# Performance work log

Measured on AMD Instinct MI355X. Metric: run time of the kernel, lower is better.

## Reference

```python
import jax, jax.numpy as jnp
import numpy as np

NH = 1024
NV = 31
LAYERS = 2
BS = 64
SEQ = 512
EPS = 1e-5


def _gru_layer(x_seq, h0, Wih, Whh, bih, bhh):
    """x_seq: [B,S,in], h0: [B,nh]. PyTorch GRU gate math. Returns [B,S,nh], h_last."""
    # Precompute input-side gates for all timesteps: [B,S,3nh]
    xg = jnp.einsum('bsi,gi->bsg', x_seq, Wih) + bih
    xg = jnp.swapaxes(xg, 0, 1)  # [S,B,3nh] for scan over time

    def step(h, xg_t):
        hg = h @ Whh.T + bhh  # [B,3nh]
        xr, xz, xn = jnp.split(xg_t, 3, axis=-1)
        hr, hz, hn = jnp.split(hg, 3, axis=-1)
        r = jax.nn.sigmoid(xr + hr)
        z = jax.nn.sigmoid(xz + hz)
        n = jnp.tanh(xn + r * hn)
        h_new = (1.0 - z) * n + z * h
        return h_new, h_new

    h_last, ys = jax.lax.scan(step, h0, xg)
    return jnp.swapaxes(ys, 0, 1), h_last  # [B,S,nh]


def setup_inputs() -> dict:
    key = jax.random.key(0)
    ks = jax.random.split(key, 16)
    s = 0.02
    inp = {
        'x': jax.random.randint(ks[0], (BS, SEQ), 0, NV),
        'h0': jnp.zeros((LAYERS, BS, NH), jnp.float32),
        'emb': jax.random.normal(ks[1], (NV, NH), jnp.float32) * s,
        'Wih0': jax.random.normal(ks[2], (3 * NH, NH), jnp.float32) * s,
        'Whh0': jax.random.normal(ks[3], (3 * NH, NH), jnp.float32) * s,
        'bih0': jnp.zeros((3 * NH,), jnp.float32),
        'bhh0': jnp.zeros((3 * NH,), jnp.float32),
        'Wih1': jax.random.normal(ks[4], (3 * NH, NH), jnp.float32) * s,
        'Whh1': jax.random.normal(ks[5], (3 * NH, NH), jnp.float32) * s,
        'bih1': jnp.zeros((3 * NH,), jnp.float32),
        'bhh1': jnp.zeros((3 * NH,), jnp.float32),
        'gamma': jnp.ones((NH,), jnp.float32),
        'beta': jnp.zeros((NH,), jnp.float32),
        'Wout': jax.random.normal(ks[6], (NV, NH), jnp.float32) * s,
        'bout': jnp.zeros((NV,), jnp.float32),
    }
    return inp


def reference(x, h0, emb, Wih0, Whh0, bih0, bhh0, Wih1, Whh1, bih1, bhh1,
              gamma, beta, Wout, bout):
    e = emb[x]  # [B,S,nh] embedding lookup
    y0, _ = _gru_layer(e, h0[0], Wih0, Whh0, bih0, bhh0)
    y1, _ = _gru_layer(y0, h0[1], Wih1, Whh1, bih1, bhh1)
    # BatchNorm1dFlat: flatten (B*S, nh), batch-statistics BN, reshape back
    flat = y1.reshape(-1, NH)
    mu = flat.mean(axis=0)
    var = flat.var(axis=0)  # biased, as in BN training
    bn = (y1 - mu) * jax.lax.rsqrt(var + EPS) * gamma + beta
    return bn @ Wout.T + bout  # [B,S,nv]
```

## Files before the change

### kernel.cpp

```cpp
#include <hip/hip_runtime.h>
#include <cstddef>
#include <stdint.h>

#define NHID 1024
#define NVOC 31
#define NB   64
#define NSEQ 512
#define NWRK 192
#define NGRID 256
#define NTHR 512
#define EPSV 1e-5f
#define RS2  36
#define SL   (NB*NHID)
#define XG_SLOTS 16

typedef __attribute__((ext_vector_type(8))) short short8;
typedef __attribute__((ext_vector_type(4))) float float4v;

#define OFF_F0  0
#define OFF_F1  4096
#define OFF_F2  8192
#define OFF_FIN 12288
#define CNT_BYTES 12352

#define M_OFF_Y0  12544
#define M_OFF_Y1  (M_OFF_Y0 + 513ull*SL*2)
#define M_OFF_H1I (M_OFF_Y1 + 512ull*SL*2)
#define M_OFF_T0  (M_OFF_H1I + (unsigned long long)SL*2)
#define M_OFF_ST  (M_OFF_T0 + 31ull*3*NHID*4)
#define M_OFF_XG  (M_OFF_ST + 16384ull)

#define LDS_BYTES 65024

__device__ __forceinline__ unsigned short f2bf(float f){
  unsigned u = __builtin_bit_cast(unsigned, f);
  u += 0x7fffu + ((u >> 16) & 1u);
  return (unsigned short)(u >> 16);
}
__device__ __forceinline__ float bf2f(unsigned short h){
  unsigned u = ((unsigned)h) << 16;
  return __builtin_bit_cast(float, u);
}
__device__ __forceinline__ float sigm(float x){ return 1.f/(1.f + __expf(-x)); }
__device__ __forceinline__ float tanh_f(float x){ return 1.f - 2.f/(__expf(2.f*x) + 1.f); }

__device__ __forceinline__ void burn(float& d){
#pragma unroll
  for (int i=0;i<16;++i)
    asm volatile("v_fmac_f32 %0, %1, %2" : "+v"(d) : "v"(d), "v"(d));
}

__device__ __forceinline__ void setflag(unsigned* f, unsigned v){
  __hip_atomic_store(f, v, __ATOMIC_RELAXED, __HIP_MEMORY_SCOPE_AGENT);
}
__device__ __forceinline__ void waitflags4(const unsigned* f, int base4, int target, int lane, float& d){
  const unsigned* p = f + (size_t)(base4 + (lane & 3))*16;
  for(;;){
    int v = (int)__hip_atomic_load(p, __ATOMIC_RELAXED, __HIP_MEMORY_SCOPE_AGENT);
    if (__all(v >= target)) break;
    burn(d);
  }
  asm volatile("" ::: "memory");
}
__device__ __forceinline__ void waitflag1(const unsigned* f, int idx, int target, float& d){
  const unsigned* p = f + (size_t)idx*16;
  while ((int)__hip_atomic_load(p, __ATOMIC_RELAXED, __HIP_MEMORY_SCOPE_AGENT) < target)
    burn(d);
  asm volatile("" ::: "memory");
}
__device__ __forceinline__ void waitflag1_slow(const unsigned* f, int idx, int target, float& d){
  const unsigned* p = f + (size_t)idx*16;
  while ((int)__hip_atomic_load(p, __ATOMIC_RELAXED, __HIP_MEMORY_SCOPE_AGENT) < target){
    burn(d); burn(d); burn(d); burn(d);
  }
  asm volatile("" ::: "memory");
}
__device__ __forceinline__ void sig(unsigned* c){
  __hip_atomic_fetch_add(c, 1u, __ATOMIC_RELAXED, __HIP_MEMORY_SCOPE_AGENT);
}
__device__ __forceinline__ void waitc(unsigned* c, unsigned v, float& d){
  while (__hip_atomic_load(c, __ATOMIC_RELAXED, __HIP_MEMORY_SCOPE_AGENT) < v)
    burn(d);
}

__device__ __forceinline__ void stc16(void* p, short8 v){
  asm volatile("global_store_dwordx4 %0, %1, off sc1"
               :: "v"((unsigned long long)(uintptr_t)p), "v"(v) : "memory");
}
__device__ __forceinline__ void stc4(void* p, float v){
  asm volatile("global_store_dword %0, %1, off sc1"
               :: "v"((unsigned long long)(uintptr_t)p), "v"(v) : "memory");
}
__device__ __forceinline__ void drain_vm(){
  asm volatile("s_waitcnt vmcnt(0)" ::: "memory");
}

__device__ __forceinline__ void load_bfrags6(const float* W, int ch0,
                                             short8 (&bfr)[6][4], int lane, int wid)
{
  const int l15 = lane & 15, q = lane >> 4;
#pragma unroll
  for (int nt=0; nt<6; ++nt){
    int grow = (nt>>1)*NHID + ch0 + (nt&1)*16 + l15;
    const float* wp0 = W + (size_t)grow*NHID + wid*128 + q*8;
#pragma unroll
    for (int kt=0; kt<4; ++kt){
      const float* wp = wp0 + kt*32;
      short8 fr;
#pragma unroll
      for (int j=0;j<8;++j) fr[j] = (short)f2bf(wp[j]);
      bfr[nt][kt] = fr;
    }
  }
}
__device__ __forceinline__ void load_a2(const unsigned short* slab, int b0,
                                        short8 (&f)[2][4], int lane, int wid)
{
#pragma unroll
  for (int mt=0;mt<2;++mt){
    const short8* p = (const short8*)(slab + (size_t)(b0 + mt*16 + (lane&15))*NHID
                                      + wid*128 + (lane>>4)*8);
#pragma unroll
    for (int kt=0;kt<4;++kt) f[mt][kt] = p[kt*4];
  }
}
__device__ __forceinline__ void gemm2d(const short8 (&fA)[2][4],
                                       const short8 (&bfr)[6][4],
                                       float* red, int lane, int wid)
{
  const int l15 = lane & 15, q = lane >> 4;
  float4v acc[2][6];
#pragma unroll
  for (int mt=0; mt<2; ++mt)
#pragma unroll
    for (int nt=0; nt<6; ++nt) acc[mt][nt] = (float4v){0.f,0.f,0.f,0.f};
#pragma unroll
  for (int kt=0; kt<4; ++kt){
#pragma unroll
    for (int nt=0; nt<6; ++nt){
      acc[0][nt] = __builtin_amdgcn_mfma_f32_16x16x32_bf16(fA[0][kt], bfr[nt][kt], acc[0][nt],0,0,0);
      acc[1][nt] = __builtin_amdgcn_mfma_f32_16x16x32_bf16(fA[1][kt], bfr[nt][kt], acc[1][nt],0,0,0);
    }
  }
  if (wid >= 4){
#pragma unroll
    for (int mt=0; mt<2; ++mt)
#pragma unroll
      for (int nt=0; nt<6; ++nt){
        int n = nt*16 + l15, row = mt*16 + q*4;
        *(float4v*)(red + ((wid-4)*96 + n)*RS2 + row) = acc[mt][nt];
      }
  }
  __syncthreads();
  if (wid < 4){
#pragma unroll
    for (int mt=0; mt<2; ++mt)
#pragma unroll
      for (int nt=0; nt<6; ++nt){
        int n = nt*16 + l15, row = mt*16 + q*4;
        float4v* p = (float4v*)(red + (wid*96 + n)*RS2 + row);
        float4v v = *p;
        *p = v + acc[mt][nt];
      }
  }
  __syncthreads();
}

__global__ __launch_bounds__(NTHR, 2) void mgru_fused(
    const int*   __restrict__ x,    const float* __restrict__ h0,
    const float* __restrict__ emb,
    const float* __restrict__ Wih0, const float* __restrict__ Whh0,
    const float* __restrict__ bih0, const float* __restrict__ bhh0,
    const float* __restrict__ Wih1, const float* __restrict__ Whh1,
    const float* __restrict__ bih1, const float* __restrict__ bhh1,
    const float* __restrict__ gamma, const float* __restrict__ beta,
    const float* __restrict__ Wout, const float* __restrict__ bout,
    float* __restrict__ out, char* ws)
{
  __shared__ __align__(16) char smem[LDS_BYTES];
  float* red = (float*)smem;

  unsigned* f0  = (unsigned*)(ws + OFF_F0);
  unsigned* f1  = (unsigned*)(ws + OFF_F1);
  unsigned* f2  = (unsigned*)(ws + OFF_F2);
  unsigned* fin = (unsigned*)(ws + OFF_FIN);
  unsigned short* y0b   = (unsigned short*)(ws + M_OFF_Y0);
  unsigned short* y1    = (unsigned short*)(ws + M_OFF_Y1);
  unsigned short* h1i   = (unsigned short*)(ws + M_OFF_H1I);
  float*          T0    = (float*)(ws + M_OFF_T0);
  float*          stats = (float*)(ws + M_OFF_ST);
  float*          xgring= (float*)(ws + M_OFF_XG);

  const int tid  = threadIdx.x;
  const int lane = tid & 63;
  const int wid  = tid >> 6;
  const int wg   = blockIdx.x;
  const int l15 = lane & 15, q = lane >> 4;
  float dummy = (float)tid * 1e-30f + 1.0f;

  if (wg >= NWRK){
    for(;;){
      for (int i=0;i<64;++i) burn(dummy);
      unsigned v = __hip_atomic_load(fin, __ATOMIC_RELAXED, __HIP_MEMORY_SCOPE_AGENT);
      if (v >= (unsigned)NWRK) break;
    }
    if (tid == 0) __threadfence();
    __syncthreads();
    if (dummy == 1234.5678f) ((volatile float*)smem)[0] = dummy;
    goto epilogue;
  }

  {
    if (tid == 0) __threadfence();
    __syncthreads();

    const int role = (wg < 64) ? 0 : (wg < 128 ? 1 : 2);

    if (role == 0){
      const int rw = wg, bg = rw >> 5, cg = rw & 31;
      const int b0 = bg*32, ch0 = cg*32;
      const int fidx = bg*32 + cg;
      const int g = tid;
      const int b = b0 + (g & 31);
      const int oct = g >> 5;
      short8 bfr0[6][4];
      float hprev[8] = {0,0,0,0,0,0,0,0};
      float br[8], bz[8], bn[8];

      if (tid < 128){
        short8 pk;
#pragma unroll
        for (int j=0;j<8;++j){
          int ch = ch0 + oct*8 + j;
          hprev[j] = h0[(size_t)b*NHID + ch];
          br[j] = bhh0[ch]; bz[j] = bhh0[NHID + ch]; bn[j] = bhh0[2*NHID + ch];
          pk[j] = (short)f2bf(hprev[j]);
        }
        stc16(y0b + (size_t)b*NHID + ch0 + oct*8, pk);
        drain_vm();
      }
      __syncthreads();
      if (tid == 0) setflag(f0 + (size_t)fidx*16, 1u);

      for (int e = tid; e < NVOC*96; e += NTHR){
        int v = e / 96, n = e - v*96;
        int gate = n >> 5, c32 = n & 31;
        int grow = gate*NHID + ch0 + c32;
        const float4v* e4 = (const float4v*)(emb  + (size_t)v*NHID);
        const float4v* w4 = (const float4v*)(Wih0 + (size_t)grow*NHID);
        float acc = 0.f;
        for (int k=0;k<NHID/4;++k){
          float4v a = e4[k], bb = w4[k];
          acc += a[0]*bb[0] + a[1]*bb[1] + a[2]*bb[2] + a[3]*bb[3];
        }
        T0[(size_t)v*3*NHID + grow] = acc + bih0[grow];
      }
      load_bfrags6(Whh0, ch0, bfr0, lane, wid);
      __syncthreads();

      for (int t = 0; t < NSEQ; ++t){
        waitflags4(f0, bg*32 + wid*4, t+1, lane, dummy);
        short8 fA[2][4];
        load_a2(y0b + (size_t)t*SL, b0, fA, lane, wid);
        gemm2d(fA, bfr0, red, lane, wid);
        if (tid < 128){
          int tok = x[(size_t)b*NSEQ + t];
          const float* tp = T0 + (size_t)tok*3*NHID;
          int m = g & 31;
          short8 pk;
#pragma unroll
          for (int j=0;j<8;++j){
            int c32 = oct*8 + j, ch = ch0 + c32;
            float hr = br[j], hz = bz[j], hn = bn[j];
#pragma unroll
            for (int w=0;w<4;++w){
              hr += red[(w*96 +      c32)*RS2 + m];
              hz += red[(w*96 + 32 + c32)*RS2 + m];
              hn += red[(w*96 + 64 + c32)*RS2 + m];
            }
            float r = sigm(tp[ch] + hr);
            float z = sigm(tp[NHID + ch] + hz);
            float n = tanh_f(tp[2*NHID + ch] + r*hn);
            float hnv = (1.f - z)*n + z*hprev[j];
            hprev[j] = hnv;
            pk[j] = (short)f2bf(hnv);
          }
          stc16(y0b + (size_t)(t+1)*SL + (size_t)b*NHID + ch0 + oct*8, pk);
          drain_vm();
        }
        __syncthreads();
        if (tid == 0) setflag(f0 + (size_t)fidx*16, (unsigned)(t+2));
      }

    } else if (role == 1){
      const int rw = wg - 64, bg = rw >> 5, cg = rw & 31;
      const int b0 = bg*32, ch0 = cg*32;
      const int fidx = bg*32 + cg;
      short8 wf[6][4];
      load_bfrags6(Wih1, ch0, wf, lane, wid);
      __syncthreads();

      for (int t = 0; t < NSEQ; ++t){
        if ((t & 3) == 0 && t >= 16)
          waitflag1_slow(f2, fidx, t-11, dummy);
        waitflags4(f0, bg*32 + wid*4, t+2, lane, dummy);
        short8 fB[2][4];
        load_a2(y0b + (size_t)(t+1)*SL, b0, fB, lane, wid);
        gemm2d(fB, wf, red, lane, wid);
        float* xgw = xgring + ((size_t)(t & (XG_SLOTS-1))*64 + (size_t)fidx)*3072;
#pragma unroll
        for (int i=0;i<6;++i){
          int idx = tid + i*512;
          int n = idx >> 5, m = idx & 31;
          float v = bih1[(n>>5)*NHID + ch0 + (n&31)];
          v += red[(      n)*RS2 + m];
          v += red[( 96 + n)*RS2 + m];
          v += red[(192 + n)*RS2 + m];
          v += red[(288 + n)*RS2 + m];
          stc4(xgw + idx, v);
        }
        drain_vm();
        __syncthreads();
        if (tid == 0) setflag(f1 + (size_t)fidx*16, (unsigned)(t+2));
      }

    } else {
      const int rw = wg - 128, bg = rw >> 5, cg = rw & 31;
      const int b0 = bg*32, ch0 = cg*32;
      const int fidx = bg*32 + cg;
      const int g = tid;
      const int b = b0 + (g & 31);
      const int oct = g >> 5;
      short8 bfrH[6][4];
      float hprev[8] = {0,0,0,0,0,0,0,0};
      float bhr[8], bhz[8], bhn[8];
      float s1[8] = {0,0,0,0,0,0,0,0}, s2[8] = {0,0,0,0,0,0,0,0};

      if (tid < 128){
        short8 pk;
#pragma unroll
        for (int j=0;j<8;++j){
          int ch = ch0 + oct*8 + j;
          hprev[j] = h0[(size_t)NB*NHID + (size_t)b*NHID + ch];
          bhr[j] = bhh1[ch]; bhz[j] = bhh1[NHID + ch]; bhn[j] = bhh1[2*NHID + ch];
          pk[j] = (short)f2bf(hprev[j]);
        }
        stc16(h1i + (size_t)b*NHID + ch0 + oct*8, pk);
        drain_vm();
      }
      __syncthreads();
      if (tid == 0) setflag(f2 + (size_t)fidx*16, 1u);

      load_bfrags6(Whh1, ch0, bfrH, lane, wid);
      __syncthreads();

      for (int t = 0; t < NSEQ; ++t){
        waitflags4(f2, bg*32 + wid*4, t+1, lane, dummy);
        const unsigned short* hsrc = (t == 0) ? h1i : (y1 + (size_t)(t-1)*SL);
        short8 fH[2][4];
        load_a2(hsrc, b0, fH, lane, wid);
        gemm2d(fH, bfrH, red, lane, wid);
        float hrv[8], hzv[8], hnv_[8];
        if (tid < 128){
          int m = g & 31;
#pragma unroll
          for (int j=0;j<8;++j){
            int c32 = oct*8 + j;
            float hr = bhr[j], hz = bhz[j], hn = bhn[j];
#pragma unroll
            for (int w=0;w<4;++w){
              hr += red[(w*96 +      c32)*RS2 + m];
              hz += red[(w*96 + 32 + c32)*RS2 + m];
              hn += red[(w*96 + 64 + c32)*RS2 + m];
            }
            hrv[j] = hr; hzv[j] = hz; hnv_[j] = hn;
          }
        }
        waitflag1(f1, fidx, t+2, dummy);
        if (tid < 128){
          const float* xgt = xgring + ((size_t)(t & (XG_SLOTS-1))*64 + (size_t)fidx)*3072;
          int m = g & 31;
          short8 pk;
#pragma unroll
          for (int j=0;j<8;++j){
            int c32 = oct*8 + j;
            float xr = __hip_atomic_load(xgt + (size_t)(     c32)*32 + m, __ATOMIC_RELAXED, __HIP_MEMORY_SCOPE_AGENT);
            float xz = __hip_atomic_load(xgt + (size_t)(32 + c32)*32 + m, __ATOMIC_RELAXED, __HIP_MEMORY_SCOPE_AGENT);
            float xn = __hip_atomic_load(xgt + (size_t)(64 + c32)*32 + m, __ATOMIC_RELAXED, __HIP_MEMORY_SCOPE_AGENT);
            float r  = sigm(xr + hrv[j]);
            float z  = sigm(xz + hzv[j]);
            float nn = tanh_f(xn + r*hnv_[j]);
            float hnew = (1.f - z)*nn + z*hprev[j];
            hprev[j] = hnew;
            unsigned short hb = f2bf(hnew);
            pk[j] = (short)hb;
            float hq = bf2f(hb);
            s1[j] += hq; s2[j] += hq*hq;
          }
          stc16(y1 + (size_t)t*SL + (size_t)b*NHID + ch0 + oct*8, pk);
          drain_vm();
        }
        __syncthreads();
        if (tid == 0) setflag(f2 + (size_t)fidx*16, (unsigned)(t+2));
      }

      {
        float* sb = (float*)smem;
        __syncthreads();
        if (tid < 128){
#pragma unroll
          for (int j=0;j<8;++j) sb[(oct*8 + j)*32 + (g & 31)] = s1[j];
        }
        __syncthreads();
        if (tid < 32){
          float a = 0.f;
          for (int i=0;i<32;++i) a += sb[tid*32 + i];
          stats[(size_t)bg*2048 + ch0 + tid] = a;
        }
        __syncthreads();
        if (tid < 128){
#pragma unroll
          for (int j=0;j<8;++j) sb[(oct*8 + j)*32 + (g & 31)] = s2[j];
        }
        __syncthreads();
        if (tid < 32){
          float a = 0.f;
          for (int i=0;i<32;++i) a += sb[tid*32 + i];
          stats[(size_t)bg*2048 + 1024 + ch0 + tid] = a;
        }
      }
    }

    __syncthreads();
    if (tid == 0){
      __threadfence();
      sig(fin);
      waitc(fin, NWRK, dummy);
      __threadfence();
    }
    __syncthreads();
    if (dummy == 1234.5678f) ((volatile float*)smem)[0] = dummy;
  }

epilogue:
  {
    const float inv_n = 1.f/32768.f;

    float* bpart    = (float*)smem;
    float* bprime_l = (float*)(smem + 2048);
    {
      int v = tid >> 4, k0 = tid & 15;
      float partial = 0.f;
      if (v < NVOC){
        for (int k = k0; k < NHID; k += 16){
          float s1k = stats[k] + stats[2048 + k];
          float s2k = stats[1024 + k] + stats[3072 + k];
          float mu  = s1k*inv_n;
          float var = s2k*inv_n - mu*mu;
          float sc  = gamma[k]*rsqrtf(var + EPSV);
          partial += (beta[k] - mu*sc) * Wout[(size_t)v*NHID + k];
        }
      }
      bpart[tid] = partial;
    }
    __syncthreads();
    if (tid < 32){
      float bpv = 0.f;
      for (int j=0;j<16;++j) bpv += bpart[tid*16 + j];
      bprime_l[tid] = (tid < NVOC) ? (bpv + bout[tid]) : 0.f;
    }
    __syncthreads();
    float bp_a = bprime_l[l15];
    float bp_b = (l15 < 15) ? bprime_l[16 + l15] : 0.f;
    __syncthreads();

    unsigned short* wsc = (unsigned short*)smem;
    for (int e = tid; e < NVOC*1032; e += NTHR){
      int v = e / 1032, k = e - v*1032;
      float val = 0.f;
      if (k < NHID){
        float s1k = stats[k] + stats[2048 + k];
        float s2k = stats[1024 + k] + stats[3072 + k];
        float mu  = s1k*inv_n;
        float var = s2k*inv_n - mu*mu;
        float sc  = gamma[k]*rsqrtf(var + EPSV);
        val = Wout[(size_t)v*NHID + k] * sc;
      }
      wsc[e] = f2bf(val);
    }
    __syncthreads();

    unsigned short* y1b = (unsigned short*)(ws + M_OFF_Y1);
    int wglob = wg*8 + wid;
    if ((wglob & 3) == 0){
      int J = wglob >> 2;
      float4v acc[4][2];
#pragma unroll
      for (int mt=0;mt<4;++mt){ acc[mt][0] = (float4v){0,0,0,0}; acc[mt][1] = (float4v){0,0,0,0}; }
      const unsigned short* abase = y1b + (size_t)(J*64 + l15)*NHID + q*8;
      const short8 zero8 = (short8){0,0,0,0,0,0,0,0};
#pragma unroll 4
      for (int kt=0; kt<32; ++kt){
        short8 bv0 = *(const short8*)(wsc + (size_t)l15*1032 + kt*32 + q*8);
        short8 bv1 = (l15 < 15) ? *(const short8*)(wsc + (size_t)(16+l15)*1032 + kt*32 + q*8) : zero8;
        short8 a0 = *(const short8*)(abase + (size_t)kt*32);
        short8 a1 = *(const short8*)(abase + 16*NHID + (size_t)kt*32);
        short8 a2 = *(const short8*)(abase + 32*NHID + (size_t)kt*32);
        short8 a3 = *(const short8*)(abase + 48*NHID + (size_t)kt*32);
        acc[0][0] = __builtin_amdgcn_mfma_f32_16x16x32_bf16(a0, bv0, acc[0][0],0,0,0);
        acc[1][0] = __builtin_amdgcn_mfma_f32_16x16x32_bf16(a1, bv0, acc[1][0],0,0,0);
        acc[2][0] = __builtin_amdgcn_mfma_f32_16x16x32_bf16(a2, bv0, acc[2][0],0,0,0);
        acc[3][0] = __builtin_amdgcn_mfma_f32_16x16x32_bf16(a3, bv0, acc[3][0],0,0,0);
        acc[0][1] = __builtin_amdgcn_mfma_f32_16x16x32_bf16(a0, bv1, acc[0][1],0,0,0);
        acc[1][1] = __builtin_amdgcn_mfma_f32_16x16x32_bf16(a1, bv1, acc[1][1],0,0,0);
        acc[2][1] = __builtin_amdgcn_mfma_f32_16x16x32_bf16(a2, bv1, acc[2][1],0,0,0);
        acc[3][1] = __builtin_amdgcn_mfma_f32_16x16x32_bf16(a3, bv1, acc[3][1],0,0,0);
      }
#pragma unroll
      for (int mt=0;mt<4;++mt){
#pragma unroll
        for (int nt=0;nt<2;++nt){
          int v = nt*16 + l15;
          if (v < NVOC){
            float bpv = (nt==0) ? bp_a : bp_b;
            int r0 = J*64 + mt*16 + q*4;
#pragma unroll
            for (int i2=0;i2<4;++i2){
              int r = r0 + i2;
              int bb = r & 63, tt = r >> 6;
              out[(size_t)(bb*NSEQ + tt)*NVOC + v] = acc[mt][nt][i2] + bpv;
            }
          }
        }
      }
    }
  }
}

extern "C" void kernel_launch(void* const* d_in, const int* in_sizes, int n_in,
                              void* d_out, int out_size, void* d_ws, size_t ws_size,
                              hipStream_t stream) {
  (void)in_sizes; (void)n_in; (void)out_size; (void)ws_size;
  hipMemsetAsync(d_ws, 0, CNT_BYTES, stream);
  mgru_fused<<<dim3(NGRID), dim3(NTHR), 0, stream>>>(
      (const int*)d_in[0],  (const float*)d_in[1],  (const float*)d_in[2],
      (const float*)d_in[3], (const float*)d_in[4], (const float*)d_in[5],
      (const float*)d_in[6], (const float*)d_in[7], (const float*)d_in[8],
      (const float*)d_in[9], (const float*)d_in[10], (const float*)d_in[11],
      (const float*)d_in[12], (const float*)d_in[13], (const float*)d_in[14],
      (float*)d_out, (char*)d_ws);
}
```

Before: 3.912 ms.

## Feed own hidden-state slice from LDS and replace block barrier with counter

In both recurrent roles, each workgroup now keeps its own freshly computed hidden-state slice in shared memory. The one warp whose K-chunk matches that slice reads it from LDS instead of waiting on its own global flag and reloading from global memory. The end-of-step __syncthreads before the flag set is replaced by an LDS atomic counter that thread 0 spins on. Next-step A fragments are prefetched right after the flag wait, so waves can start loading as soon as their peers' flags arrive. This shortens the serial per-timestep critical path, at the cost of more complex intra-block ordering that relies on the LDS counter and a block fence.

```diff
diff --git a/kernel.cpp b/kernel.cpp
--- a/kernel.cpp
+++ b/kernel.cpp
@@ -30,6 +30,8 @@
 #define M_OFF_ST  (M_OFF_T0 + 31ull*3*NHID*4)
 #define M_OFF_XG  (M_OFF_ST + 16384ull)
 
+#define OWN_OFF   55296
+#define CNT_OFF   (OWN_OFF + 2560)
 #define LDS_BYTES 65024
 
 __device__ __forceinline__ unsigned short f2bf(float f){
@@ -53,14 +55,21 @@
 __device__ __forceinline__ void setflag(unsigned* f, unsigned v){
   __hip_atomic_store(f, v, __ATOMIC_RELAXED, __HIP_MEMORY_SCOPE_AGENT);
 }
-__device__ __forceinline__ void waitflags4(const unsigned* f, int base4, int target, int lane, float& d){
-  const unsigned* p = f + (size_t)(base4 + (lane & 3))*16;
+__device__ __forceinline__ void waitflags4_skip(const unsigned* f, int base4, int skip,
+                                                int target, int lane, float& d){
+  int fi = lane & 3;
+  const unsigned* p = f + (size_t)(base4 + fi)*16;
+  bool active = (fi != skip);
   for(;;){
-    int v = (int)__hip_atomic_load(p, __ATOMIC_RELAXED, __HIP_MEMORY_SCOPE_AGENT);
+    int v = active ? (int)__hip_atomic_load(p, __ATOMIC_RELAXED, __HIP_MEMORY_SCOPE_AGENT)
+                   : 0x7fffffff;
     if (__all(v >= target)) break;
     burn(d);
   }
   asm volatile("" ::: "memory");
+}
+__device__ __forceinline__ void waitflags4(const unsigned* f, int base4, int target, int lane, float& d){
+  waitflags4_skip(f, base4, -1, target, lane, d);
 }
 __device__ __forceinline__ void waitflag1(const unsigned* f, int idx, int target, float& d){
   const unsigned* p = f + (size_t)idx*16;
@@ -122,6 +131,22 @@
                                       + wid*128 + (lane>>4)*8);
 #pragma unroll
     for (int kt=0;kt<4;++kt) f[mt][kt] = p[kt*4];
+  }
+}
+__device__ __forceinline__ void load_a2_mixed(const unsigned short* slab, int b0,
+                                              const unsigned short* ownb, int skip,
+                                              short8 (&f)[2][4], int lane, int wid)
+{
+#pragma unroll
+  for (int mt=0;mt<2;++mt){
+    const unsigned short* rowg = slab + (size_t)(b0 + mt*16 + (lane&15))*NHID
+                                 + wid*128 + (lane>>4)*8;
+    const unsigned short* rowl = ownb + (size_t)(mt*16 + (lane&15))*40 + (lane>>4)*8;
+#pragma unroll
+    for (int kt=0;kt<4;++kt){
+      f[mt][kt] = (kt == skip) ? *(const short8*)rowl
+                               : *(const short8*)(rowg + kt*32);
+    }
   }
 }
 __device__ __forceinline__ void gemm2d(const short8 (&fA)[2][4],
@@ -179,6 +204,8 @@
 {
   __shared__ __align__(16) char smem[LDS_BYTES];
   float* red = (float*)smem;
+  unsigned short* ownb = (unsigned short*)(smem + OWN_OFF);
+  unsigned* lcnt = (unsigned*)(smem + CNT_OFF);
 
   unsigned* f0  = (unsigned*)(ws + OFF_F0);
   unsigned* f1  = (unsigned*)(ws + OFF_F1);
@@ -211,7 +238,7 @@
   }
 
   {
-    if (tid == 0) __threadfence();
+    if (tid == 0){ __threadfence(); *lcnt = 0u; }
     __syncthreads();
 
     const int role = (wg < 64) ? 0 : (wg < 128 ? 1 : 2);
@@ -223,6 +250,7 @@
       const int g = tid;
       const int b = b0 + (g & 31);
       const int oct = g >> 5;
+      const int skip = (wid == (cg>>2)) ? (cg&3) : -1;
       short8 bfr0[6][4];
       float hprev[8] = {0,0,0,0,0,0,0,0};
       float br[8], bz[8], bn[8];
@@ -237,6 +265,7 @@
           pk[j] = (short)f2bf(hprev[j]);
         }
         stc16(y0b + (size_t)b*NHID + ch0 + oct*8, pk);
+        *(short8*)(ownb + (size_t)(g & 31)*40 + oct*8) = pk;
         drain_vm();
       }
       __syncthreads();
@@ -258,10 +287,12 @@
       load_bfrags6(Whh0, ch0, bfr0, lane, wid);
       __syncthreads();
 
+      short8 fA[2][4];
+      waitflags4_skip(f0, bg*32 + wid*4, skip, 1, lane, dummy);
+      load_a2_mixed(y0b, b0, ownb, skip, fA, lane, wid);
+
       for (int t = 0; t < NSEQ; ++t){
-        waitflags4(f0, bg*32 + wid*4, t+1, lane, dummy);
-        short8 fA[2][4];
-        load_a2(y0b + (size_t)t*SL, b0, fA, lane, wid);
+        __syncthreads();
         gemm2d(fA, bfr0, red, lane, wid);
         if (tid < 128){
           int tok = x[(size_t)b*NSEQ + t];
@@ -286,10 +317,23 @@
             pk[j] = (short)f2bf(hnv);
           }
           stc16(y0b + (size_t)(t+1)*SL + (size_t)b*NHID + ch0 + oct*8, pk);
+          *(short8*)(ownb + (size_t)m*40 + oct*8) = pk;
+          __threadfence_block();
           drain_vm();
-        }
-        __syncthreads();
-        if (tid == 0) setflag(f0 + (size_t)fidx*16, (unsigned)(t+2));
+          __hip_atomic_fetch_add(lcnt, 1u, __ATOMIC_RELAXED, __HIP_MEMORY_SCOPE_WORKGROUP);
+          if (tid == 0){
+            while (__hip_atomic_load(lcnt, __ATOMIC_RELAXED, __HIP_MEMORY_SCOPE_WORKGROUP) < 128u*(unsigned)(t+1)) {}
+            setflag(f0 + (size_t)fidx*16, (unsigned)(t+2));
+          }
+        }
+        if (t+1 < NSEQ){
+          waitflags4_skip(f0, bg*32 + wid*4, skip, t+2, lane, dummy);
+          if (skip >= 0){
+            while (__hip_atomic_load(lcnt, __ATOMIC_RELAXED, __HIP_MEMORY_SCOPE_WORKGROUP) < 128u*(unsigned)(t+1)) burn(dummy);
+            asm volatile("" ::: "memory");
+          }
+          load_a2_mixed(y0b + (size_t)(t+1)*SL, b0, ownb, skip, fA, lane, wid);
+        }
       }
 
     } else if (role == 1){
@@ -331,6 +375,7 @@
       const int g = tid;
       const int b = b0 + (g & 31);
       const int oct = g >> 5;
+      const int skip = (wid == (cg>>2)) ? (cg&3) : -1;
       short8 bfrH[6][4];
       float hprev[8] = {0,0,0,0,0,0,0,0};
       float bhr[8], bhz[8], bhn[8];
@@ -346,6 +391,7 @@
           pk[j] = (short)f2bf(hprev[j]);
         }
         stc16(h1i + (size_t)b*NHID + ch0 + oct*8, pk);
+        *(short8*)(ownb + (size_t)(g & 31)*40 + oct*8) = pk;
         drain_vm();
       }
       __syncthreads();
@@ -354,15 +400,16 @@
       load_bfrags6(Whh1, ch0, bfrH, lane, wid);
       __syncthreads();
 
+      short8 fH[2][4];
+      waitflags4_skip(f2, bg*32 + wid*4, skip, 1, lane, dummy);
+      load_a2_mixed(h1i, b0, ownb, skip, fH, lane, wid);
+
       for (int t = 0; t < NSEQ; ++t){
-        waitflags4(f2, bg*32 + wid*4, t+1, lane, dummy);
-        const unsigned short* hsrc = (t == 0) ? h1i : (y1 + (size_t)(t-1)*SL);
-        short8 fH[2][4];
-        load_a2(hsrc, b0, fH, lane, wid);
+        __syncthreads();
         gemm2d(fH, bfrH, red, lane, wid);
-        float hrv[8], hzv[8], hnv_[8];
         if (tid < 128){
           int m = g & 31;
+          float hrv[8], hzv[8], hnv_[8];
 #pragma unroll
           for (int j=0;j<8;++j){
             int c32 = oct*8 + j;
@@ -375,11 +422,8 @@
             }
             hrv[j] = hr; hzv[j] = hz; hnv_[j] = hn;
           }
-        }
-        waitflag1(f1, fidx, t+2, dummy);
-        if (tid < 128){
+          waitflag1(f1, fidx, t+2, dummy);
           const float* xgt = xgring + ((size_t)(t & (XG_SLOTS-1))*64 + (size_t)fidx)*3072;
-          int m = g & 31;
           short8 pk;
 #pragma unroll
           for (int j=0;j<8;++j){
@@ -398,10 +442,23 @@
             s1[j] += hq; s2[j] += hq*hq;
           }
           stc16(y1 + (size_t)t*SL + (size_t)b*NHID + ch0 + oct*8, pk);
+          *(short8*)(ownb + (size_t)m*40 + oct*8) = pk;
+          __threadfence_block();
           drain_vm();
-        }
-        __syncthreads();
-        if (tid == 0) setflag(f2 + (size_t)fidx*16, (unsigned)(t+2));
+          __hip_atomic_fetch_add(lcnt, 1u, __ATOMIC_RELAXED, __HIP_MEMORY_SCOPE_WORKGROUP);
+          if (tid == 0){
+            while (__hip_atomic_load(lcnt, __ATOMIC_RELAXED, __HIP_MEMORY_SCOPE_WORKGROUP) < 128u*(unsigned)(t+1)) {}
+            setflag(f2 + (size_t)fidx*16, (unsigned)(t+2));
+          }
+        }
+        if (t+1 < NSEQ){
+          waitflags4_skip(f2, bg*32 + wid*4, skip, t+2, lane, dummy);
+          if (skip >= 0){
+            while (__hip_atomic_load(lcnt, __ATOMIC_RELAXED, __HIP_MEMORY_SCOPE_WORKGROUP) < 128u*(unsigned)(t+1)) burn(dummy);
+            asm volatile("" ::: "memory");
+          }
+          load_a2_mixed(y1 + (size_t)t*SL, b0, ownb, skip, fH, lane, wid);
+        }
       }
 
       {
```

Result: slower. 5.669 ms (+44.9%).
